# Performance work log

Measured on AMD Instinct MI355X. Metric: run time of the kernel, lower is better.

## Reference

```python
import jax, jax.numpy as jnp
import numpy as np

EPS = 1e-7
MAX_TANH = 15.0
C = 1.0  # curvature of every PoincareBall manifold in the stack

def _norm(x):
    return jnp.clip(jnp.linalg.norm(x, axis=-1, keepdims=True), EPS, None)

def _artanh(x):
    return jnp.arctanh(jnp.clip(x, -1.0 + 1e-5, 1.0 - 1e-5))

def proj(x, c=C):
    # clip points back inside the Poincare ball
    maxnorm = (1.0 - 1e-5) / jnp.sqrt(c)
    n = _norm(x)
    return jnp.where(n > maxnorm, x / n * maxnorm, x)

def expmap0(u, c=C):
    sc = jnp.sqrt(c)
    n = _norm(u)
    return jnp.tanh(jnp.clip(sc * n, -MAX_TANH, MAX_TANH)) * u / (sc * n)

def logmap0(x, c=C):
    sc = jnp.sqrt(c)
    n = _norm(x)
    return _artanh(sc * n) * x / (sc * n)

def mobius_add(x, y, c=C):
    x2 = jnp.sum(x * x, -1, keepdims=True)
    y2 = jnp.sum(y * y, -1, keepdims=True)
    xy = jnp.sum(x * y, -1, keepdims=True)
    num = (1 + 2 * c * xy + c * y2) * x + (1 - c * x2) * y
    den = 1 + 2 * c * xy + c * c * x2 * y2
    return num / jnp.clip(den, EPS, None)

def mobius_matvec(W, x, c=C):
    sc = jnp.sqrt(c)
    xn = _norm(x)
    mx = x @ W.T
    mxn = _norm(mx)
    return jnp.tanh(jnp.clip(mxn / xn * _artanh(sc * xn), -MAX_TANH, MAX_TANH)) * mx / (mxn * sc)

def hgc_layer(x, edges, node_mask, edge_mask, W, b, c_in=C, c_out=C):
    n_nodes = x.shape[0]
    # HypLinear: mobius matvec + hyperbolic bias add
    h = proj(mobius_matvec(W, x, c_in), c_in)
    hyp_bias = proj(expmap0(b[None, :], c_in), c_in)
    h = proj(mobius_add(h, hyp_bias, c_in), c_in)
    # HypAgg: masked tangent-space mean over incoming edges (gather -> segment_sum)
    row, col = edges[0], edges[1]
    ht = logmap0(h, c_in)                 # [N, d] tangent features
    msgs = ht[col] * edge_mask            # [E, d]
    agg = jax.ops.segment_sum(msgs, row, num_segments=n_nodes)
    deg = jax.ops.segment_sum(edge_mask, row, num_segments=n_nodes)
    agg = agg / jnp.clip(deg, 1.0, None)
    h = proj(expmap0(agg, c_in), c_in)
    # HypAct: nonlinearity in tangent space, re-map to output manifold
    xt = jax.nn.relu(logmap0(h, c_in))
    h = proj(expmap0(xt, c_out), c_out)
    return h * node_mask

N_NODES = 50000
N_EDGES = 1200000
DIM = 64
NUM_LAYERS = 2

def setup_inputs() -> dict:
    key = jax.random.key(0)
    ks = jax.random.split(key, 8)
    h_tan = 0.1 * jax.random.normal(ks[0], (N_NODES, DIM), dtype=jnp.float32)
    h = proj(expmap0(h_tan))  # valid Poincare-ball points
    distances = jax.random.uniform(ks[1], (N_EDGES, 1), dtype=jnp.float32)
    edges = jax.random.randint(ks[2], (2, N_EDGES), 0, N_NODES, dtype=jnp.int64)
    node_mask = jnp.ones((N_NODES, 1), dtype=jnp.float32)
    edge_mask = jnp.ones((N_EDGES, 1), dtype=jnp.float32)
    W0 = 0.1 * jax.random.normal(ks[3], (DIM, DIM), dtype=jnp.float32)
    b0 = 0.01 * jax.random.normal(ks[4], (DIM,), dtype=jnp.float32)
    W1 = 0.1 * jax.random.normal(ks[5], (DIM, DIM), dtype=jnp.float32)
    b1 = 0.01 * jax.random.normal(ks[6], (DIM,), dtype=jnp.float32)
    return {"h": h, "distances": distances, "edges": edges,
            "node_mask": node_mask, "edge_mask": edge_mask,
            "W0": W0, "b0": b0, "W1": W1, "b1": b1}

def reference(h, distances, edges, node_mask, edge_mask, W0, b0, W1, b1):
    # nn.Sequential of HyperbolicGraphConvolution layers; distances/edges/masks pass through
    out = hgc_layer(h, edges, node_mask, edge_mask, W0, b0)
    out = hgc_layer(out, edges, node_mask, edge_mask, W1, b1)
    return out
```

## Files before the change

### kernel.cpp

```cpp
#include <hip/hip_runtime.h>
#include <hip/hip_fp16.h>

#define EPS      1e-7f
#define MAX_TANH 15.0f
#define MAXNORM  0.99999f
#define ART_CLIP 0.99999f
#define HGRID    512
#define RPB      64
#define RPB_SHIFT 6
#define CAPF     2048
#define NBMAX    1024

__device__ __forceinline__ float wave_sum64(float v) {
#pragma unroll
    for (int o = 32; o > 0; o >>= 1) v += __shfl_xor(v, o, 64);
    return v;
}

__device__ __forceinline__ float gsum16(float v) {
    v += __shfl_xor(v, 1, 64);
    v += __shfl_xor(v, 2, 64);
    v += __shfl_xor(v, 4, 64);
    v += __shfl_xor(v, 8, 64);
    return v;
}

__device__ __forceinline__ float clamp_tanh_arg(float x) {
    return fminf(fmaxf(x, -MAX_TANH), MAX_TANH);
}

__device__ __forceinline__ float artanh_clip(float x) {
    x = fminf(fmaxf(x, -ART_CLIP), ART_CLIP);
    return 0.5f * logf((1.0f + x) / (1.0f - x));
}

__device__ __forceinline__ void fma_h4(float4& acc, uint2 u, float m) {
    float2 f01 = __half22float2(*reinterpret_cast<__half2*>(&u.x));
    float2 f23 = __half22float2(*reinterpret_cast<__half2*>(&u.y));
    acc.x = fmaf(f01.x, m, acc.x); acc.y = fmaf(f01.y, m, acc.y);
    acc.z = fmaf(f23.x, m, acc.z); acc.w = fmaf(f23.y, m, acc.w);
}

__global__ __launch_bounds__(256) void hist_transform_kernel(
    const int* __restrict__ rows, unsigned short* __restrict__ histB,
    int n_edges, int epb, int nb,
    const float* __restrict__ x, const float* __restrict__ W,
    const float* __restrict__ b, __half* __restrict__ ht, int n_nodes)
{
    __shared__ float WT[4096];
    __shared__ float xs[16 * 68];
    __shared__ int hh[NBMAX];

    if (blockIdx.x < HGRID) {
        const int b0 = blockIdx.x * epb;
        const int b1 = min(b0 + epb, n_edges);
        for (int j = threadIdx.x; j < nb; j += 256) hh[j] = 0;
        __syncthreads();
        for (int i = b0 + threadIdx.x; i < b1; i += 256)
            atomicAdd(&hh[rows[i] >> RPB_SHIFT], 1);
        __syncthreads();
        for (int j = threadIdx.x; j < nb; j += 256)
            histB[blockIdx.x * nb + j] = (unsigned short)hh[j];
        return;
    }

    const int t = threadIdx.x;
    const int q = t & 15;
    const int g = t >> 4;
    const int bid = blockIdx.x - HGRID;
    const int tgrid = gridDim.x - HGRID;

#pragma unroll
    for (int r = 0; r < 16; ++r) {
        int idx = r * 256 + t;
        int j = idx >> 6, k = idx & 63;
        WT[(k << 6) | (j ^ ((k & 15) << 2))] = W[idx];
    }

    float4 b4 = ((const float4*)b)[q];
    float ssb = b4.x*b4.x + b4.y*b4.y + b4.z*b4.z + b4.w*b4.w;
    float bn = fmaxf(sqrtf(gsum16(ssb)), EPS);
    float tb = tanhf(clamp_tanh_arg(bn));
    float sb = tb / bn;
    float4 hb4 = make_float4(b4.x * sb, b4.y * sb, b4.z * sb, b4.w * sb);
    if (tb > MAXNORM) {
        float sc = MAXNORM / tb;
        hb4.x *= sc; hb4.y *= sc; hb4.z *= sc; hb4.w *= sc;
        tb = MAXNORM;
    }
    const float y2 = tb * tb;
    __syncthreads();

    float* xrow = &xs[g * 68];

    for (int base = bid * 16; base < n_nodes; base += tgrid * 16) {
        const int node = base + g;
        const bool valid = node < n_nodes;
        const int nd = valid ? node : 0;

        float4 x4 = ((const float4*)(x + (long long)nd * 64))[q];
        *(float4*)(xrow + (q << 2)) = x4;

        float ssx = x4.x*x4.x + x4.y*x4.y + x4.z*x4.z + x4.w*x4.w;
        float xn = fmaxf(sqrtf(gsum16(ssx)), EPS);

        float4 mxa = make_float4(0.f, 0.f, 0.f, 0.f);
        float4 mxb = make_float4(0.f, 0.f, 0.f, 0.f);
#pragma unroll
        for (int k = 0; k < 64; k += 2) {
            float xk0 = xrow[k], xk1 = xrow[k + 1];
            const float4 w0 = *(const float4*)&WT[((k    ) << 6) | ((q << 2) ^ (((k    ) & 15) << 2))];
            const float4 w1 = *(const float4*)&WT[((k + 1) << 6) | ((q << 2) ^ (((k + 1) & 15) << 2))];
            mxa.x = fmaf(w0.x, xk0, mxa.x); mxa.y = fmaf(w0.y, xk0, mxa.y);
            mxa.z = fmaf(w0.z, xk0, mxa.z); mxa.w = fmaf(w0.w, xk0, mxa.w);
            mxb.x = fmaf(w1.x, xk1, mxb.x); mxb.y = fmaf(w1.y, xk1, mxb.y);
            mxb.z = fmaf(w1.z, xk1, mxb.z); mxb.w = fmaf(w1.w, xk1, mxb.w);
        }
        float4 mx = make_float4(mxa.x + mxb.x, mxa.y + mxb.y,
                                mxa.z + mxb.z, mxa.w + mxb.w);

        float ssm = mx.x*mx.x + mx.y*mx.y + mx.z*mx.z + mx.w*mx.w;
        float mxn = fmaxf(sqrtf(gsum16(ssm)), EPS);
        float r = tanhf(clamp_tanh_arg(mxn / xn * artanh_clip(xn)));
        float rs = r / mxn;
        float4 hj = make_float4(mx.x * rs, mx.y * rs, mx.z * rs, mx.w * rs);
        float hn = fmaxf(r, EPS);
        if (hn > MAXNORM) {
            float sc = MAXNORM / hn;
            hj.x *= sc; hj.y *= sc; hj.z *= sc; hj.w *= sc;
            hn = MAXNORM;
        }

        float x2 = hn * hn;
        float xy = gsum16(hj.x*hb4.x + hj.y*hb4.y + hj.z*hb4.z + hj.w*hb4.w);
        float ca = 1.0f + 2.0f * xy + y2;
        float cb = 1.0f - x2;
        float iden = 1.0f / fmaxf(1.0f + 2.0f * xy + x2 * y2, EPS);
        hj.x = (ca * hj.x + cb * hb4.x) * iden;
        hj.y = (ca * hj.y + cb * hb4.y) * iden;
        hj.z = (ca * hj.z + cb * hb4.z) * iden;
        hj.w = (ca * hj.w + cb * hb4.w) * iden;

        float ssh = hj.x*hj.x + hj.y*hj.y + hj.z*hj.z + hj.w*hj.w;
        float hn2 = fmaxf(sqrtf(gsum16(ssh)), EPS);
        float sc2 = (hn2 > MAXNORM) ? (MAXNORM / hn2) : 1.0f;
        float hnc = fminf(hn2, MAXNORM);
        float lr = artanh_clip(hnc) / hnc * sc2;
        hj.x *= lr; hj.y *= lr; hj.z *= lr; hj.w *= lr;

        if (valid) {
            __half2 p01 = __float22half2_rn(make_float2(hj.x, hj.y));
            __half2 p23 = __float22half2_rn(make_float2(hj.z, hj.w));
            uint2 o;
            o.x = *reinterpret_cast<unsigned*>(&p01);
            o.y = *reinterpret_cast<unsigned*>(&p23);
            *((uint2*)(ht + (long long)node * 64) + q) = o;
        }
    }
}

__global__ __launch_bounds__(HGRID) void scan_bucket_kernel(
    unsigned short* __restrict__ histB, int* __restrict__ tot, int nb)
{
    __shared__ int wsum[8];
    const int b = blockIdx.x;
    const int t = threadIdx.x;
    const int lane = t & 63, wid = t >> 6;
    int v = histB[t * nb + b];
    int incl = v;
#pragma unroll
    for (int o = 1; o < 64; o <<= 1) {
        int tt = __shfl_up(incl, o, 64);
        if (lane >= o) incl += tt;
    }
    if (lane == 63) wsum[wid] = incl;
    __syncthreads();
    if (wid == 0 && lane < 8) {
        int ws = wsum[lane];
#pragma unroll
        for (int o = 1; o < 8; o <<= 1) {
            int tt = __shfl_up(ws, o, 64);
            if (lane >= o) ws += tt;
        }
        wsum[lane] = ws;
    }
    __syncthreads();
    int base = (wid > 0) ? wsum[wid - 1] : 0;
    histB[t * nb + b] = (unsigned short)(base + incl - v);
    if (t == HGRID - 1) tot[b] = base + incl;
}

__global__ __launch_bounds__(NBMAX) void scan_base_kernel(
    const int* __restrict__ tot, int* __restrict__ bucket_base, int nb)
{
    __shared__ int s[NBMAX];
    const int t = threadIdx.x;
    int v = (t < nb) ? tot[t] : 0;
    s[t] = v;
    __syncthreads();
    for (int off = 1; off < NBMAX; off <<= 1) {
        int u = (t >= off) ? s[t - off] : 0;
        __syncthreads();
        s[t] += u;
        __syncthreads();
    }
    if (t < nb) bucket_base[t] = s[t] - v;
    if (t == nb - 1) bucket_base[nb] = s[t];
}

__global__ __launch_bounds__(256) void coarse_scatter_kernel(
    const int* __restrict__ rows, const int* __restrict__ cols,
    const float* __restrict__ edge_mask, const unsigned short* __restrict__ off,
    const int* __restrict__ bucket_base,
    int2* __restrict__ coarse, int n_edges, int epb, int nb)
{
    __shared__ int cur[NBMAX];
    const int b0 = blockIdx.x * epb;
    const int b1 = min(b0 + epb, n_edges);
    for (int j = threadIdx.x; j < nb; j += 256)
        cur[j] = bucket_base[j] + (int)off[blockIdx.x * nb + j];
    __syncthreads();
    for (int i = b0 + threadIdx.x; i < b1; i += 256) {
        int r = rows[i], c = cols[i];
        float m = edge_mask[i];
        int pos = atomicAdd(&cur[r >> RPB_SHIFT], 1);
        coarse[pos] = make_int2((r << 16) | c, __float_as_int(m));
    }
}

__global__ __launch_bounds__(512) void fine_gather_kernel(
    const int2* __restrict__ coarse, const int* __restrict__ bucket_base,
    const __half* __restrict__ ht1, const float* __restrict__ node_mask,
    const float* __restrict__ W, const float* __restrict__ bvec,
    unsigned* __restrict__ csr4, int* __restrict__ row_start,
    __half* __restrict__ ht2, int n_nodes, int n_edges)
{
    __shared__ int hh[RPB], incl[RPB], curs[RPB];
    __shared__ int2 outE[CAPF];
    __shared__ float WT[4096];
    __shared__ float xs[32 * 68];

    const int t = threadIdx.x;
    const int b = blockIdx.x;
    const int q = t & 15;
    const int g = t >> 4;
    const int bbase = bucket_base[b];
    const int n_e = bucket_base[b + 1] - bbase;

#pragma unroll
    for (int r = 0; r < 8; ++r) {
        int idx = r * 512 + t;
        int j = idx >> 6, k = idx & 63;
        WT[(k << 6) | (j ^ ((k & 15) << 2))] = W[idx];
    }
    float4 b4 = ((const float4*)bvec)[q];
    float ssb = b4.x*b4.x + b4.y*b4.y + b4.z*b4.z + b4.w*b4.w;
    float bn = fmaxf(sqrtf(gsum16(ssb)), EPS);
    float tb = tanhf(clamp_tanh_arg(bn));
    float sb = tb / bn;
    float4 hb4 = make_float4(b4.x * sb, b4.y * sb, b4.z * sb, b4.w * sb);
    if (tb > MAXNORM) {
        float sc = MAXNORM / tb;
        hb4.x *= sc; hb4.y *= sc; hb4.z *= sc; hb4.w *= sc;
        tb = MAXNORM;
    }
    const float y2 = tb * tb;

    if (t < RPB) hh[t] = 0;
    __syncthreads();
    int2 regs[4];
#pragma unroll
    for (int k = 0; k < 4; ++k) {
        int i = t + k * 512;
        if (i < n_e) {
            regs[k] = coarse[bbase + i];
            atomicAdd(&hh[(regs[k].x >> 16) & (RPB - 1)], 1);
        }
    }
    __syncthreads();
    if (t < 64) {
        int v = hh[t];
        int inc = v;
#pragma unroll
        for (int o = 1; o < 64; o <<= 1) {
            int tt = __shfl_up(inc, o, 64);
            if (t >= o) inc += tt;
        }
        incl[t] = inc;
        curs[t] = inc - v;
        int grow = (b << RPB_SHIFT) + t;
        if (grow < n_nodes) row_start[grow] = bbase + inc - v;
    }
    if (b == gridDim.x - 1 && t == 0) row_start[n_nodes] = n_edges;
    __syncthreads();
#pragma unroll
    for (int k = 0; k < 4; ++k) {
        int i = t + k * 512;
        if (i < n_e) {
            int slot = atomicAdd(&curs[(regs[k].x >> 16) & (RPB - 1)], 1);
            if (slot < CAPF) outE[slot] = make_int2(regs[k].x & 0xffff, regs[k].y);
        }
    }
    __syncthreads();

    const int lim = min(n_e, CAPF);
    for (int i = t; i < lim; i += 512) {
        int2 rec = outE[i];
        __half hm = __float2half(__int_as_float(rec.y));
        csr4[bbase + i] = (unsigned)rec.x |
                          ((unsigned)*reinterpret_cast<unsigned short*>(&hm) << 16);
    }

    const uint2* __restrict__ htq = (const uint2*)ht1 + q;

#pragma unroll
    for (int batch = 0; batch < 2; ++batch) {
        const int ln = batch * 32 + g;
        const int node = (b << RPB_SHIFT) + ln;
        const bool valid = node < n_nodes;
        const int nd = valid ? node : (n_nodes - 1);
        const int s0 = incl[ln] - hh[ln];
        const int e0 = incl[ln];

        float4 acc = make_float4(0.f, 0.f, 0.f, 0.f);
        float msum = 0.f;
        int j = s0;
        for (; j + 8 <= e0; j += 8) {
            int2 r0 = outE[j    ], r1 = outE[j + 1], r2 = outE[j + 2], r3 = outE[j + 3];
            int2 r4 = outE[j + 4], r5 = outE[j + 5], r6 = outE[j + 6], r7 = outE[j + 7];
            uint2 u0 = htq[(unsigned)r0.x * 16u];
            uint2 u1 = htq[(unsigned)r1.x * 16u];
            uint2 u2 = htq[(unsigned)r2.x * 16u];
            uint2 u3 = htq[(unsigned)r3.x * 16u];
            uint2 u4 = htq[(unsigned)r4.x * 16u];
            uint2 u5 = htq[(unsigned)r5.x * 16u];
            uint2 u6 = htq[(unsigned)r6.x * 16u];
            uint2 u7 = htq[(unsigned)r7.x * 16u];
            float m0 = __int_as_float(r0.y), m1 = __int_as_float(r1.y);
            float m2 = __int_as_float(r2.y), m3 = __int_as_float(r3.y);
            float m4 = __int_as_float(r4.y), m5 = __int_as_float(r5.y);
            float m6 = __int_as_float(r6.y), m7 = __int_as_float(r7.y);
            fma_h4(acc, u0, m0); fma_h4(acc, u1, m1);
            fma_h4(acc, u2, m2); fma_h4(acc, u3, m3);
            fma_h4(acc, u4, m4); fma_h4(acc, u5, m5);
            fma_h4(acc, u6, m6); fma_h4(acc, u7, m7);
            msum += (m0 + m1 + m2 + m3) + (m4 + m5 + m6 + m7);
        }
        for (; j + 4 <= e0; j += 4) {
            int2 r0 = outE[j], r1 = outE[j + 1], r2 = outE[j + 2], r3 = outE[j + 3];
            uint2 u0 = htq[(unsigned)r0.x * 16u];
            uint2 u1 = htq[(unsigned)r1.x * 16u];
            uint2 u2 = htq[(unsigned)r2.x * 16u];
            uint2 u3 = htq[(unsigned)r3.x * 16u];
            float m0 = __int_as_float(r0.y), m1 = __int_as_float(r1.y);
            float m2 = __int_as_float(r2.y), m3 = __int_as_float(r3.y);
            fma_h4(acc, u0, m0); fma_h4(acc, u1, m1);
            fma_h4(acc, u2, m2); fma_h4(acc, u3, m3);
            msum += m0 + m1 + m2 + m3;
        }
        for (; j < e0; ++j) {
            int2 rec = outE[j];
            uint2 u = htq[(unsigned)rec.x * 16u];
            float m = __int_as_float(rec.y);
            fma_h4(acc, u, m);
            msum += m;
        }

        const float inv = 1.0f / fmaxf(msum, 1.0f);
        acc.x *= inv; acc.y *= inv; acc.z *= inv; acc.w *= inv;

        float ss = acc.x*acc.x + acc.y*acc.y + acc.z*acc.z + acc.w*acc.w;
        float n1 = fmaxf(sqrtf(gsum16(ss)), EPS);
        float t1 = tanhf(clamp_tanh_arg(n1));
        float r1 = t1 / n1;
        acc.x *= r1; acc.y *= r1; acc.z *= r1; acc.w *= r1;
        if (t1 > MAXNORM) {
            float sc = MAXNORM / t1;
            acc.x *= sc; acc.y *= sc; acc.z *= sc; acc.w *= sc;
            t1 = MAXNORM;
        }
        float n2 = fmaxf(t1, EPS);
        float r2s = artanh_clip(n2) / n2;
        acc.x = fmaxf(acc.x * r2s, 0.f); acc.y = fmaxf(acc.y * r2s, 0.f);
        acc.z = fmaxf(acc.z * r2s, 0.f); acc.w = fmaxf(acc.w * r2s, 0.f);

        ss = acc.x*acc.x + acc.y*acc.y + acc.z*acc.z + acc.w*acc.w;
        float n3 = fmaxf(sqrtf(gsum16(ss)), EPS);
        float t3 = tanhf(clamp_tanh_arg(n3));
        float r3 = t3 / n3;
        acc.x *= r3; acc.y *= r3; acc.z *= r3; acc.w *= r3;
        if (t3 > MAXNORM) {
            float sc = MAXNORM / t3;
            acc.x *= sc; acc.y *= sc; acc.z *= sc; acc.w *= sc;
            t3 = MAXNORM;
        }

        const float nm = node_mask[nd];
        acc.x *= nm; acc.y *= nm; acc.z *= nm; acc.w *= nm;

        float* xrow = &xs[g * 68];
        *(float4*)(xrow + (q << 2)) = acc;

        float4 mxa = make_float4(0.f, 0.f, 0.f, 0.f);
        float4 mxb = make_float4(0.f, 0.f, 0.f, 0.f);
#pragma unroll
        for (int k = 0; k < 64; k += 2) {
            float xk0 = xrow[k], xk1 = xrow[k + 1];
            const float4 w0 = *(const float4*)&WT[((k    ) << 6) | ((q << 2) ^ (((k    ) & 15) << 2))];
            const float4 w1 = *(const float4*)&WT[((k + 1) << 6) | ((q << 2) ^ (((k + 1) & 15) << 2))];
            mxa.x = fmaf(w0.x, xk0, mxa.x); mxa.y = fmaf(w0.y, xk0, mxa.y);
            mxa.z = fmaf(w0.z, xk0, mxa.z); mxa.w = fmaf(w0.w, xk0, mxa.w);
            mxb.x = fmaf(w1.x, xk1, mxb.x); mxb.y = fmaf(w1.y, xk1, mxb.y);
            mxb.z = fmaf(w1.z, xk1, mxb.z); mxb.w = fmaf(w1.w, xk1, mxb.w);
        }
        float4 mx = make_float4(mxa.x + mxb.x, mxa.y + mxb.y,
                                mxa.z + mxb.z, mxa.w + mxb.w);

        float xn  = fmaxf(t3 * fabsf(nm), EPS);
        float ssm = mx.x*mx.x + mx.y*mx.y + mx.z*mx.z + mx.w*mx.w;
        float mxn = fmaxf(sqrtf(gsum16(ssm)), EPS);
        float r = tanhf(clamp_tanh_arg(mxn / xn * artanh_clip(xn)));
        float rs = r / mxn;
        float4 hj = make_float4(mx.x * rs, mx.y * rs, mx.z * rs, mx.w * rs);
        float hn = fmaxf(r, EPS);
        if (hn > MAXNORM) {
            float sc = MAXNORM / hn;
            hj.x *= sc; hj.y *= sc; hj.z *= sc; hj.w *= sc;
            hn = MAXNORM;
        }

        float x2 = hn * hn;
        float xy = gsum16(hj.x*hb4.x + hj.y*hb4.y + hj.z*hb4.z + hj.w*hb4.w);
        float ca = 1.0f + 2.0f * xy + y2;
        float cb = 1.0f - x2;
        float iden = 1.0f / fmaxf(1.0f + 2.0f * xy + x2 * y2, EPS);
        hj.x = (ca * hj.x + cb * hb4.x) * iden;
        hj.y = (ca * hj.y + cb * hb4.y) * iden;
        hj.z = (ca * hj.z + cb * hb4.z) * iden;
        hj.w = (ca * hj.w + cb * hb4.w) * iden;

        float ssh = hj.x*hj.x + hj.y*hj.y + hj.z*hj.z + hj.w*hj.w;
        float hn2 = fmaxf(sqrtf(gsum16(ssh)), EPS);
        float sc2 = (hn2 > MAXNORM) ? (MAXNORM / hn2) : 1.0f;
        float hnc = fminf(hn2, MAXNORM);
        float lr = artanh_clip(hnc) / hnc * sc2;
        hj.x *= lr; hj.y *= lr; hj.z *= lr; hj.w *= lr;

        if (valid) {
            __half2 p01 = __float22half2_rn(make_float2(hj.x, hj.y));
            __half2 p23 = __float22half2_rn(make_float2(hj.z, hj.w));
            uint2 o;
            o.x = *reinterpret_cast<unsigned*>(&p01);
            o.y = *reinterpret_cast<unsigned*>(&p23);
            *((uint2*)(ht2 + (long long)node * 64) + q) = o;
        }
    }
}

__global__ __launch_bounds__(256) void gather2_kernel(
    const __half* __restrict__ ht, const unsigned* __restrict__ csr4,
    const int* __restrict__ row_start, const float* __restrict__ node_mask,
    float* __restrict__ outp, int n_nodes)
{
    const int t = threadIdx.x;
    const int lane = t & 63;
    const int wv = t >> 6;
    const int ns = lane >> 4;
    const int q  = lane & 15;

    const int node = blockIdx.x * 16 + (wv << 2) + ns;
    const bool valid = node < n_nodes;
    const int nd = valid ? node : (n_nodes - 1);
    const int s = row_start[nd];
    const int e = row_start[nd + 1];

    const uint2* __restrict__ htq = (const uint2*)ht + q;

    float4 acc = make_float4(0.f, 0.f, 0.f, 0.f);
    float msum = 0.f;
    int j = s;
    for (; j + 8 <= e; j += 8) {
        unsigned v0 = csr4[j    ], v1 = csr4[j + 1], v2 = csr4[j + 2], v3 = csr4[j + 3];
        unsigned v4 = csr4[j + 4], v5 = csr4[j + 5], v6 = csr4[j + 6], v7 = csr4[j + 7];
        uint2 u0 = htq[(v0 & 0xffffu) * 16u];
        uint2 u1 = htq[(v1 & 0xffffu) * 16u];
        uint2 u2 = htq[(v2 & 0xffffu) * 16u];
        uint2 u3 = htq[(v3 & 0xffffu) * 16u];
        uint2 u4 = htq[(v4 & 0xffffu) * 16u];
        uint2 u5 = htq[(v5 & 0xffffu) * 16u];
        uint2 u6 = htq[(v6 & 0xffffu) * 16u];
        uint2 u7 = htq[(v7 & 0xffffu) * 16u];
        unsigned short h0 = v0 >> 16, h1 = v1 >> 16, h2 = v2 >> 16, h3 = v3 >> 16;
        unsigned short h4 = v4 >> 16, h5 = v5 >> 16, h6 = v6 >> 16, h7 = v7 >> 16;
        float m0 = __half2float(*reinterpret_cast<__half*>(&h0));
        float m1 = __half2float(*reinterpret_cast<__half*>(&h1));
        float m2 = __half2float(*reinterpret_cast<__half*>(&h2));
        float m3 = __half2float(*reinterpret_cast<__half*>(&h3));
        float m4 = __half2float(*reinterpret_cast<__half*>(&h4));
        float m5 = __half2float(*reinterpret_cast<__half*>(&h5));
        float m6 = __half2float(*reinterpret_cast<__half*>(&h6));
        float m7 = __half2float(*reinterpret_cast<__half*>(&h7));
        fma_h4(acc, u0, m0); fma_h4(acc, u1, m1);
        fma_h4(acc, u2, m2); fma_h4(acc, u3, m3);
        fma_h4(acc, u4, m4); fma_h4(acc, u5, m5);
        fma_h4(acc, u6, m6); fma_h4(acc, u7, m7);
        msum += (m0 + m1 + m2 + m3) + (m4 + m5 + m6 + m7);
    }
    for (; j + 4 <= e; j += 4) {
        unsigned v0 = csr4[j], v1 = csr4[j + 1], v2 = csr4[j + 2], v3 = csr4[j + 3];
        uint2 u0 = htq[(v0 & 0xffffu) * 16u];
        uint2 u1 = htq[(v1 & 0xffffu) * 16u];
        uint2 u2 = htq[(v2 & 0xffffu) * 16u];
        uint2 u3 = htq[(v3 & 0xffffu) * 16u];
        unsigned short h0 = v0 >> 16, h1 = v1 >> 16, h2 = v2 >> 16, h3 = v3 >> 16;
        float m0 = __half2float(*reinterpret_cast<__half*>(&h0));
        float m1 = __half2float(*reinterpret_cast<__half*>(&h1));
        float m2 = __half2float(*reinterpret_cast<__half*>(&h2));
        float m3 = __half2float(*reinterpret_cast<__half*>(&h3));
        fma_h4(acc, u0, m0); fma_h4(acc, u1, m1);
        fma_h4(acc, u2, m2); fma_h4(acc, u3, m3);
        msum += m0 + m1 + m2 + m3;
    }
    for (; j < e; ++j) {
        unsigned v = csr4[j];
        uint2 u = htq[(v & 0xffffu) * 16u];
        unsigned short hb = v >> 16;
        float m = __half2float(*reinterpret_cast<__half*>(&hb));
        fma_h4(acc, u, m);
        msum += m;
    }

    const float inv = 1.0f / fmaxf(msum, 1.0f);
    acc.x *= inv; acc.y *= inv; acc.z *= inv; acc.w *= inv;

    float ss = acc.x*acc.x + acc.y*acc.y + acc.z*acc.z + acc.w*acc.w;
    float n1 = fmaxf(sqrtf(gsum16(ss)), EPS);
    float t1 = tanhf(clamp_tanh_arg(n1));
    float r1 = t1 / n1;
    acc.x *= r1; acc.y *= r1; acc.z *= r1; acc.w *= r1;
    if (t1 > MAXNORM) {
        float sc = MAXNORM / t1;
        acc.x *= sc; acc.y *= sc; acc.z *= sc; acc.w *= sc;
        t1 = MAXNORM;
    }
    float n2 = fmaxf(t1, EPS);
    float r2 = artanh_clip(n2) / n2;
    acc.x = fmaxf(acc.x * r2, 0.f); acc.y = fmaxf(acc.y * r2, 0.f);
    acc.z = fmaxf(acc.z * r2, 0.f); acc.w = fmaxf(acc.w * r2, 0.f);

    ss = acc.x*acc.x + acc.y*acc.y + acc.z*acc.z + acc.w*acc.w;
    float n3 = fmaxf(sqrtf(gsum16(ss)), EPS);
    float t3 = tanhf(clamp_tanh_arg(n3));
    float r3 = t3 / n3;
    acc.x *= r3; acc.y *= r3; acc.z *= r3; acc.w *= r3;
    if (t3 > MAXNORM) {
        float sc = MAXNORM / t3;
        acc.x *= sc; acc.y *= sc; acc.z *= sc; acc.w *= sc;
        t3 = MAXNORM;
    }

    const float nm = node_mask[nd];
    acc.x *= nm; acc.y *= nm; acc.z *= nm; acc.w *= nm;

    if (valid) ((float4*)(outp + (long long)node * 64))[q] = acc;
}

extern "C" void kernel_launch(void* const* d_in, const int* in_sizes, int n_in,
                              void* d_out, int out_size, void* d_ws, size_t ws_size,
                              hipStream_t stream) {
    const float* h         = (const float*)d_in[0];
    const int*   edges     = (const int*)d_in[2];
    const float* node_mask = (const float*)d_in[3];
    const float* edge_mask = (const float*)d_in[4];
    const float* W0        = (const float*)d_in[5];
    const float* b0        = (const float*)d_in[6];
    const float* W1        = (const float*)d_in[7];
    const float* b1        = (const float*)d_in[8];
    float* out = (float*)d_out;

    const int N = in_sizes[0] / 64;
    const int E = in_sizes[4];
    const int* rows = edges;
    const int* cols = edges + E;

    const int NB  = (N + RPB - 1) / RPB;
    const int EPB = (E + HGRID - 1) / HGRID;

    size_t nd = (size_t)N * 64;
    char* ws = (char*)d_ws;
    __half*   B1          = (__half*)ws;   ws += nd * sizeof(__half);
    __half*   B2          = (__half*)ws;   ws += nd * sizeof(__half);
    int2*     coarse      = (int2*)ws;     ws += (size_t)E * sizeof(int2);
    unsigned* csr4        = (unsigned*)ws; ws += (size_t)E * sizeof(unsigned);
    unsigned short* histB = (unsigned short*)ws;
    ws += (size_t)HGRID * NB * sizeof(unsigned short);
    int*      tot         = (int*)ws;      ws += (size_t)NB * sizeof(int);
    int*      bucket_base = (int*)ws;      ws += (size_t)(NB + 1) * sizeof(int);
    int*      row_start   = (int*)ws;      ws += (size_t)(N + 1) * sizeof(int);

    const int TGRID = 2048;
    const int NGRID = (N + 15) / 16;

    hist_transform_kernel<<<HGRID + TGRID, 256, 0, stream>>>(
        rows, histB, E, EPB, NB, h, W0, b0, B1, N);

    scan_bucket_kernel<<<NB, HGRID, 0, stream>>>(histB, tot, NB);
    scan_base_kernel<<<1, NBMAX, 0, stream>>>(tot, bucket_base, NB);

    coarse_scatter_kernel<<<HGRID, 256, 0, stream>>>(
        rows, cols, edge_mask, histB, bucket_base, coarse, E, EPB, NB);

    fine_gather_kernel<<<NB, 512, 0, stream>>>(
        coarse, bucket_base, B1, node_mask, W1, b1, csr4, row_start, B2, N, E);

    gather2_kernel<<<NGRID, 256, 0, stream>>>(
        B2, csr4, row_start, node_mask, out, N);
}
```

Measured before the change: 219.8 us.

## Split histogram and transform kernels; use fast tanh, log and reciprocal intrinsics

Splits the fused histogram+transform launch into two separate kernels. The transform kernel now uses one 16-node tile per block instead of a grid-stride loop, launched with enough blocks to cover all nodes and occupancy hints. Separately, tanhf, logf and divisions across all kernels are replaced by exp-based tanh, __logf and hardware rcp approximations to cut transcendental cost. This trades some accuracy for speed and adds one kernel launch, which also serializes the two formerly concurrent phases.

```diff
diff --git a/kernel.cpp b/kernel.cpp
--- a/kernel.cpp
+++ b/kernel.cpp
@@ -11,10 +11,22 @@
 #define CAPF     2048
 #define NBMAX    1024
 
-__device__ __forceinline__ float wave_sum64(float v) {
-#pragma unroll
-    for (int o = 32; o > 0; o >>= 1) v += __shfl_xor(v, o, 64);
-    return v;
+__device__ __forceinline__ float frcp(float x) {
+    return __builtin_amdgcn_rcpf(x);
+}
+
+__device__ __forceinline__ float fast_tanh_pos(float x) {
+    float e = __expf(-2.0f * x);
+    return (1.0f - e) * frcp(1.0f + e);
+}
+
+__device__ __forceinline__ float clamp_tanh_arg(float x) {
+    return fminf(fmaxf(x, -MAX_TANH), MAX_TANH);
+}
+
+__device__ __forceinline__ float artanh_clip(float x) {
+    x = fminf(fmaxf(x, -ART_CLIP), ART_CLIP);
+    return 0.5f * __logf((1.0f + x) * frcp(1.0f - x));
 }
 
 __device__ __forceinline__ float gsum16(float v) {
@@ -25,15 +37,6 @@
     return v;
 }
 
-__device__ __forceinline__ float clamp_tanh_arg(float x) {
-    return fminf(fmaxf(x, -MAX_TANH), MAX_TANH);
-}
-
-__device__ __forceinline__ float artanh_clip(float x) {
-    x = fminf(fmaxf(x, -ART_CLIP), ART_CLIP);
-    return 0.5f * logf((1.0f + x) / (1.0f - x));
-}
-
 __device__ __forceinline__ void fma_h4(float4& acc, uint2 u, float m) {
     float2 f01 = __half22float2(*reinterpret_cast<__half2*>(&u.x));
     float2 f23 = __half22float2(*reinterpret_cast<__half2*>(&u.y));
@@ -41,34 +44,32 @@
     acc.z = fmaf(f23.x, m, acc.z); acc.w = fmaf(f23.y, m, acc.w);
 }
 
-__global__ __launch_bounds__(256) void hist_transform_kernel(
+__global__ __launch_bounds__(256) void hist_kernel(
     const int* __restrict__ rows, unsigned short* __restrict__ histB,
-    int n_edges, int epb, int nb,
+    int n_edges, int epb, int nb)
+{
+    __shared__ int hh[NBMAX];
+    const int b0 = blockIdx.x * epb;
+    const int b1 = min(b0 + epb, n_edges);
+    for (int j = threadIdx.x; j < nb; j += 256) hh[j] = 0;
+    __syncthreads();
+    for (int i = b0 + threadIdx.x; i < b1; i += 256)
+        atomicAdd(&hh[rows[i] >> RPB_SHIFT], 1);
+    __syncthreads();
+    for (int j = threadIdx.x; j < nb; j += 256)
+        histB[blockIdx.x * nb + j] = (unsigned short)hh[j];
+}
+
+__global__ __launch_bounds__(256, 4) void transform_kernel(
     const float* __restrict__ x, const float* __restrict__ W,
     const float* __restrict__ b, __half* __restrict__ ht, int n_nodes)
 {
     __shared__ float WT[4096];
     __shared__ float xs[16 * 68];
-    __shared__ int hh[NBMAX];
-
-    if (blockIdx.x < HGRID) {
-        const int b0 = blockIdx.x * epb;
-        const int b1 = min(b0 + epb, n_edges);
-        for (int j = threadIdx.x; j < nb; j += 256) hh[j] = 0;
-        __syncthreads();
-        for (int i = b0 + threadIdx.x; i < b1; i += 256)
-            atomicAdd(&hh[rows[i] >> RPB_SHIFT], 1);
-        __syncthreads();
-        for (int j = threadIdx.x; j < nb; j += 256)
-            histB[blockIdx.x * nb + j] = (unsigned short)hh[j];
-        return;
-    }
 
     const int t = threadIdx.x;
     const int q = t & 15;
     const int g = t >> 4;
-    const int bid = blockIdx.x - HGRID;
-    const int tgrid = gridDim.x - HGRID;
 
 #pragma unroll
     for (int r = 0; r < 16; ++r) {
@@ -80,82 +81,80 @@
     float4 b4 = ((const float4*)b)[q];
     float ssb = b4.x*b4.x + b4.y*b4.y + b4.z*b4.z + b4.w*b4.w;
     float bn = fmaxf(sqrtf(gsum16(ssb)), EPS);
-    float tb = tanhf(clamp_tanh_arg(bn));
-    float sb = tb / bn;
+    float tb = fast_tanh_pos(clamp_tanh_arg(bn));
+    float sb = tb * frcp(bn);
     float4 hb4 = make_float4(b4.x * sb, b4.y * sb, b4.z * sb, b4.w * sb);
     if (tb > MAXNORM) {
-        float sc = MAXNORM / tb;
+        float sc = MAXNORM * frcp(tb);
         hb4.x *= sc; hb4.y *= sc; hb4.z *= sc; hb4.w *= sc;
         tb = MAXNORM;
     }
     const float y2 = tb * tb;
     __syncthreads();
 
+    const int node = blockIdx.x * 16 + g;
+    const bool valid = node < n_nodes;
+    const int nd = valid ? node : 0;
+
     float* xrow = &xs[g * 68];
 
-    for (int base = bid * 16; base < n_nodes; base += tgrid * 16) {
-        const int node = base + g;
-        const bool valid = node < n_nodes;
-        const int nd = valid ? node : 0;
-
-        float4 x4 = ((const float4*)(x + (long long)nd * 64))[q];
-        *(float4*)(xrow + (q << 2)) = x4;
-
-        float ssx = x4.x*x4.x + x4.y*x4.y + x4.z*x4.z + x4.w*x4.w;
-        float xn = fmaxf(sqrtf(gsum16(ssx)), EPS);
-
-        float4 mxa = make_float4(0.f, 0.f, 0.f, 0.f);
-        float4 mxb = make_float4(0.f, 0.f, 0.f, 0.f);
-#pragma unroll
-        for (int k = 0; k < 64; k += 2) {
-            float xk0 = xrow[k], xk1 = xrow[k + 1];
-            const float4 w0 = *(const float4*)&WT[((k    ) << 6) | ((q << 2) ^ (((k    ) & 15) << 2))];
-            const float4 w1 = *(const float4*)&WT[((k + 1) << 6) | ((q << 2) ^ (((k + 1) & 15) << 2))];
-            mxa.x = fmaf(w0.x, xk0, mxa.x); mxa.y = fmaf(w0.y, xk0, mxa.y);
-            mxa.z = fmaf(w0.z, xk0, mxa.z); mxa.w = fmaf(w0.w, xk0, mxa.w);
-            mxb.x = fmaf(w1.x, xk1, mxb.x); mxb.y = fmaf(w1.y, xk1, mxb.y);
-            mxb.z = fmaf(w1.z, xk1, mxb.z); mxb.w = fmaf(w1.w, xk1, mxb.w);
-        }
-        float4 mx = make_float4(mxa.x + mxb.x, mxa.y + mxb.y,
-                                mxa.z + mxb.z, mxa.w + mxb.w);
-
-        float ssm = mx.x*mx.x + mx.y*mx.y + mx.z*mx.z + mx.w*mx.w;
-        float mxn = fmaxf(sqrtf(gsum16(ssm)), EPS);
-        float r = tanhf(clamp_tanh_arg(mxn / xn * artanh_clip(xn)));
-        float rs = r / mxn;
-        float4 hj = make_float4(mx.x * rs, mx.y * rs, mx.z * rs, mx.w * rs);
-        float hn = fmaxf(r, EPS);
-        if (hn > MAXNORM) {
-            float sc = MAXNORM / hn;
-            hj.x *= sc; hj.y *= sc; hj.z *= sc; hj.w *= sc;
-            hn = MAXNORM;
-        }
-
-        float x2 = hn * hn;
-        float xy = gsum16(hj.x*hb4.x + hj.y*hb4.y + hj.z*hb4.z + hj.w*hb4.w);
-        float ca = 1.0f + 2.0f * xy + y2;
-        float cb = 1.0f - x2;
-        float iden = 1.0f / fmaxf(1.0f + 2.0f * xy + x2 * y2, EPS);
-        hj.x = (ca * hj.x + cb * hb4.x) * iden;
-        hj.y = (ca * hj.y + cb * hb4.y) * iden;
-        hj.z = (ca * hj.z + cb * hb4.z) * iden;
-        hj.w = (ca * hj.w + cb * hb4.w) * iden;
-
-        float ssh = hj.x*hj.x + hj.y*hj.y + hj.z*hj.z + hj.w*hj.w;
-        float hn2 = fmaxf(sqrtf(gsum16(ssh)), EPS);
-        float sc2 = (hn2 > MAXNORM) ? (MAXNORM / hn2) : 1.0f;
-        float hnc = fminf(hn2, MAXNORM);
-        float lr = artanh_clip(hnc) / hnc * sc2;
-        hj.x *= lr; hj.y *= lr; hj.z *= lr; hj.w *= lr;
-
-        if (valid) {
-            __half2 p01 = __float22half2_rn(make_float2(hj.x, hj.y));
-            __half2 p23 = __float22half2_rn(make_float2(hj.z, hj.w));
-            uint2 o;
-            o.x = *reinterpret_cast<unsigned*>(&p01);
-            o.y = *reinterpret_cast<unsigned*>(&p23);
-            *((uint2*)(ht + (long long)node * 64) + q) = o;
-        }
+    float4 x4 = ((const float4*)(x + (long long)nd * 64))[q];
+    *(float4*)(xrow + (q << 2)) = x4;
+
+    float ssx = x4.x*x4.x + x4.y*x4.y + x4.z*x4.z + x4.w*x4.w;
+    float xn = fmaxf(sqrtf(gsum16(ssx)), EPS);
+
+    float4 mxa = make_float4(0.f, 0.f, 0.f, 0.f);
+    float4 mxb = make_float4(0.f, 0.f, 0.f, 0.f);
+#pragma unroll
+    for (int k = 0; k < 64; k += 2) {
+        float xk0 = xrow[k], xk1 = xrow[k + 1];
+        const float4 w0 = *(const float4*)&WT[((k    ) << 6) | ((q << 2) ^ (((k    ) & 15) << 2))];
+        const float4 w1 = *(const float4*)&WT[((k + 1) << 6) | ((q << 2) ^ (((k + 1) & 15) << 2))];
+        mxa.x = fmaf(w0.x, xk0, mxa.x); mxa.y = fmaf(w0.y, xk0, mxa.y);
+        mxa.z = fmaf(w0.z, xk0, mxa.z); mxa.w = fmaf(w0.w, xk0, mxa.w);
+        mxb.x = fmaf(w1.x, xk1, mxb.x); mxb.y = fmaf(w1.y, xk1, mxb.y);
+        mxb.z = fmaf(w1.z, xk1, mxb.z); mxb.w = fmaf(w1.w, xk1, mxb.w);
+    }
+    float4 mx = make_float4(mxa.x + mxb.x, mxa.y + mxb.y,
+                            mxa.z + mxb.z, mxa.w + mxb.w);
+
+    float ssm = mx.x*mx.x + mx.y*mx.y + mx.z*mx.z + mx.w*mx.w;
+    float mxn = fmaxf(sqrtf(gsum16(ssm)), EPS);
+    float r = fast_tanh_pos(clamp_tanh_arg(mxn * frcp(xn) * artanh_clip(xn)));
+    float rs = r * frcp(mxn);
+    float4 hj = make_float4(mx.x * rs, mx.y * rs, mx.z * rs, mx.w * rs);
+    float hn = fmaxf(r, EPS);
+    if (hn > MAXNORM) {
+        float sc = MAXNORM * frcp(hn);
+        hj.x *= sc; hj.y *= sc; hj.z *= sc; hj.w *= sc;
+        hn = MAXNORM;
+    }
+
+    float x2 = hn * hn;
+    float xy = gsum16(hj.x*hb4.x + hj.y*hb4.y + hj.z*hb4.z + hj.w*hb4.w);
+    float ca = 1.0f + 2.0f * xy + y2;
+    float cb = 1.0f - x2;
+    float iden = frcp(fmaxf(1.0f + 2.0f * xy + x2 * y2, EPS));
+    hj.x = (ca * hj.x + cb * hb4.x) * iden;
+    hj.y = (ca * hj.y + cb * hb4.y) * iden;
+    hj.z = (ca * hj.z + cb * hb4.z) * iden;
+    hj.w = (ca * hj.w + cb * hb4.w) * iden;
+
+    float ssh = hj.x*hj.x + hj.y*hj.y + hj.z*hj.z + hj.w*hj.w;
+    float hn2 = fmaxf(sqrtf(gsum16(ssh)), EPS);
+    float sc2 = (hn2 > MAXNORM) ? (MAXNORM * frcp(hn2)) : 1.0f;
+    float hnc = fminf(hn2, MAXNORM);
+    float lr = artanh_clip(hnc) * frcp(hnc) * sc2;
+    hj.x *= lr; hj.y *= lr; hj.z *= lr; hj.w *= lr;
+
+    if (valid) {
+        __half2 p01 = __float22half2_rn(make_float2(hj.x, hj.y));
+        __half2 p23 = __float22half2_rn(make_float2(hj.z, hj.w));
+        uint2 o;
+        o.x = *reinterpret_cast<unsigned*>(&p01);
+        o.y = *reinterpret_cast<unsigned*>(&p23);
+        *((uint2*)(ht + (long long)node * 64) + q) = o;
     }
 }
 
@@ -256,11 +255,11 @@
     float4 b4 = ((const float4*)bvec)[q];
     float ssb = b4.x*b4.x + b4.y*b4.y + b4.z*b4.z + b4.w*b4.w;
     float bn = fmaxf(sqrtf(gsum16(ssb)), EPS);
-    float tb = tanhf(clamp_tanh_arg(bn));
-    float sb = tb / bn;
+    float tb = fast_tanh_pos(clamp_tanh_arg(bn));
+    float sb = tb * frcp(bn);
     float4 hb4 = make_float4(b4.x * sb, b4.y * sb, b4.z * sb, b4.w * sb);
     if (tb > MAXNORM) {
-        float sc = MAXNORM / tb;
+        float sc = MAXNORM * frcp(tb);
         hb4.x *= sc; hb4.y *= sc; hb4.z *= sc; hb4.w *= sc;
         tb = MAXNORM;
     }
@@ -366,31 +365,31 @@
             msum += m;
         }
 
-        const float inv = 1.0f / fmaxf(msum, 1.0f);
+        const float inv = frcp(fmaxf(msum, 1.0f));
         acc.x *= inv; acc.y *= inv; acc.z *= inv; acc.w *= inv;
 
         float ss = acc.x*acc.x + acc.y*acc.y + acc.z*acc.z + acc.w*acc.w;
         float n1 = fmaxf(sqrtf(gsum16(ss)), EPS);
-        float t1 = tanhf(clamp_tanh_arg(n1));
-        float r1 = t1 / n1;
+        float t1 = fast_tanh_pos(clamp_tanh_arg(n1));
+        float r1 = t1 * frcp(n1);
         acc.x *= r1; acc.y *= r1; acc.z *= r1; acc.w *= r1;
         if (t1 > MAXNORM) {
-            float sc = MAXNORM / t1;
+            float sc = MAXNORM * frcp(t1);
             acc.x *= sc; acc.y *= sc; acc.z *= sc; acc.w *= sc;
             t1 = MAXNORM;
         }
         float n2 = fmaxf(t1, EPS);
-        float r2s = artanh_clip(n2) / n2;
+        float r2s = artanh_clip(n2) * frcp(n2);
         acc.x = fmaxf(acc.x * r2s, 0.f); acc.y = fmaxf(acc.y * r2s, 0.f);
         acc.z = fmaxf(acc.z * r2s, 0.f); acc.w = fmaxf(acc.w * r2s, 0.f);
 
         ss = acc.x*acc.x + acc.y*acc.y + acc.z*acc.z + acc.w*acc.w;
         float n3 = fmaxf(sqrtf(gsum16(ss)), EPS);
-        float t3 = tanhf(clamp_tanh_arg(n3));
-        float r3 = t3 / n3;
+        float t3 = fast_tanh_pos(clamp_tanh_arg(n3));
+        float r3 = t3 * frcp(n3);
         acc.x *= r3; acc.y *= r3; acc.z *= r3; acc.w *= r3;
         if (t3 > MAXNORM) {
-            float sc = MAXNORM / t3;
+            float sc = MAXNORM * frcp(t3);
             acc.x *= sc; acc.y *= sc; acc.z *= sc; acc.w *= sc;
             t3 = MAXNORM;
         }
@@ -419,12 +418,12 @@
         float xn  = fmaxf(t3 * fabsf(nm), EPS);
         float ssm = mx.x*mx.x + mx.y*mx.y + mx.z*mx.z + mx.w*mx.w;
         float mxn = fmaxf(sqrtf(gsum16(ssm)), EPS);
-        float r = tanhf(clamp_tanh_arg(mxn / xn * artanh_clip(xn)));
-        float rs = r / mxn;
+        float r = fast_tanh_pos(clamp_tanh_arg(mxn * frcp(xn) * artanh_clip(xn)));
+        float rs = r * frcp(mxn);
         float4 hj = make_float4(mx.x * rs, mx.y * rs, mx.z * rs, mx.w * rs);
         float hn = fmaxf(r, EPS);
         if (hn > MAXNORM) {
-            float sc = MAXNORM / hn;
+            float sc = MAXNORM * frcp(hn);
             hj.x *= sc; hj.y *= sc; hj.z *= sc; hj.w *= sc;
             hn = MAXNORM;
         }
@@ -433,7 +432,7 @@
         float xy = gsum16(hj.x*hb4.x + hj.y*hb4.y + hj.z*hb4.z + hj.w*hb4.w);
         float ca = 1.0f + 2.0f * xy + y2;
         float cb = 1.0f - x2;
-        float iden = 1.0f / fmaxf(1.0f + 2.0f * xy + x2 * y2, EPS);
+        float iden = frcp(fmaxf(1.0f + 2.0f * xy + x2 * y2, EPS));
         hj.x = (ca * hj.x + cb * hb4.x) * iden;
         hj.y = (ca * hj.y + cb * hb4.y) * iden;
         hj.z = (ca * hj.z + cb * hb4.z) * iden;
@@ -441,9 +440,9 @@
 
         float ssh = hj.x*hj.x + hj.y*hj.y + hj.z*hj.z + hj.w*hj.w;
         float hn2 = fmaxf(sqrtf(gsum16(ssh)), EPS);
-        float sc2 = (hn2 > MAXNORM) ? (MAXNORM / hn2) : 1.0f;
+        float sc2 = (hn2 > MAXNORM) ? (MAXNORM * frcp(hn2)) : 1.0f;
         float hnc = fminf(hn2, MAXNORM);
-        float lr = artanh_clip(hnc) / hnc * sc2;
+        float lr = artanh_clip(hnc) * frcp(hnc) * sc2;
         hj.x *= lr; hj.y *= lr; hj.z *= lr; hj.w *= lr;
 
         if (valid) {
@@ -530,31 +529,31 @@
         msum += m;
     }
 
-    const float inv = 1.0f / fmaxf(msum, 1.0f);
+    const float inv = frcp(fmaxf(msum, 1.0f));
     acc.x *= inv; acc.y *= inv; acc.z *= inv; acc.w *= inv;
 
     float ss = acc.x*acc.x + acc.y*acc.y + acc.z*acc.z + acc.w*acc.w;
     float n1 = fmaxf(sqrtf(gsum16(ss)), EPS);
-    float t1 = tanhf(clamp_tanh_arg(n1));
-    float r1 = t1 / n1;
+    float t1 = fast_tanh_pos(clamp_tanh_arg(n1));
+    float r1 = t1 * frcp(n1);
     acc.x *= r1; acc.y *= r1; acc.z *= r1; acc.w *= r1;
     if (t1 > MAXNORM) {
-        float sc = MAXNORM / t1;
+        float sc = MAXNORM * frcp(t1);
         acc.x *= sc; acc.y *= sc; acc.z *= sc; acc.w *= sc;
         t1 = MAXNORM;
     }
     float n2 = fmaxf(t1, EPS);
-    float r2 = artanh_clip(n2) / n2;
+    float r2 = artanh_clip(n2) * frcp(n2);
     acc.x = fmaxf(acc.x * r2, 0.f); acc.y = fmaxf(acc.y * r2, 0.f);
     acc.z = fmaxf(acc.z * r2, 0.f); acc.w = fmaxf(acc.w * r2, 0.f);
 
     ss = acc.x*acc.x + acc.y*acc.y + acc.z*acc.z + acc.w*acc.w;
     float n3 = fmaxf(sqrtf(gsum16(ss)), EPS);
-    float t3 = tanhf(clamp_tanh_arg(n3));
-    float r3 = t3 / n3;
+    float t3 = fast_tanh_pos(clamp_tanh_arg(n3));
+    float r3 = t3 * frcp(n3);
     acc.x *= r3; acc.y *= r3; acc.z *= r3; acc.w *= r3;
     if (t3 > MAXNORM) {
-        float sc = MAXNORM / t3;
+        float sc = MAXNORM * frcp(t3);
         acc.x *= sc; acc.y *= sc; acc.z *= sc; acc.w *= sc;
         t3 = MAXNORM;
     }
@@ -598,11 +597,12 @@
     int*      bucket_base = (int*)ws;      ws += (size_t)(NB + 1) * sizeof(int);
     int*      row_start   = (int*)ws;      ws += (size_t)(N + 1) * sizeof(int);
 
-    const int TGRID = 2048;
+    const int TB = (N + 15) / 16;
     const int NGRID = (N + 15) / 16;
 
-    hist_transform_kernel<<<HGRID + TGRID, 256, 0, stream>>>(
-        rows, histB, E, EPB, NB, h, W0, b0, B1, N);
+    hist_kernel<<<HGRID, 256, 0, stream>>>(rows, histB, E, EPB, NB);
+
+    transform_kernel<<<TB, 256, 0, stream>>>(h, W0, b0, B1, N);
 
     scan_bucket_kernel<<<NB, HGRID, 0, stream>>>(histB, tot, NB);
     scan_base_kernel<<<1, NBMAX, 0, stream>>>(tot, bucket_base, NB);
```

New measurement: 195.9 us (median of 2 runs). 10.8% less time.
